# Kernel tuning notes

Hardware: AMD Instinct MI355X
Metric: run time of the kernel (lower is better)

The kernel has to match this reference:

```python
import jax, jax.numpy as jnp
import numpy as np

B, C, H, W_ = 16, 256, 128, 128

def setup_inputs() -> dict:
    key = jax.random.key(0)
    k1, k2 = jax.random.split(key)
    x = jax.random.normal(k1, (B, C, H, W_), dtype=jnp.float32)
    # nn.Linear(C, C): weight [C, C], bias [C]
    Wm = jax.random.normal(k2, (C, C), dtype=jnp.float32) * (1.0 / np.sqrt(C))
    b = jnp.zeros((C,), dtype=jnp.float32)
    return {"x": x, "W": Wm, "b": b}

def reference(x, W, b):
    # Channel frequency transform: mean of real(fft2) over spatial freq bins -> [B, C]
    cf = jnp.fft.fft2(x, axes=(-2, -1)).real.mean(axis=(-2, -1))
    cf = jax.nn.sigmoid(cf @ W.T + b)                       # [B, C]
    x_cft = x * cf[:, :, None, None]
    # Spatial frequency transform: fft2 of channel-mean map -> [B, H, W]
    sf = jnp.fft.fft2(x.mean(axis=1, keepdims=True), axes=(-2, -1)).real.mean(axis=1)
    x_sft = x * sf[:, None, :, :]
    return x_cft + x_sft
```

## Files before the change

### kernel.cpp

```cpp
#include <hip/hip_runtime.h>

#define Bn   16
#define Cn   256
#define Hd   128
#define Wd   128
#define HW   16384
#define HW4  4096

#define TWO_PI 6.283185307179586

#define OFF_XM   0
#define OFF_X00  262144
#define OFF_CF   266240
#define OFF_C1   270336
#define OFF_S1   532480
#define OFF_SF   794624

__global__ void k1_mean_x00(const float* __restrict__ x,
                            float* __restrict__ xm, float* __restrict__ x00) {
    int tid = blockIdx.x * blockDim.x + threadIdx.x;
    int b = tid >> 12;
    int p = tid & (HW4 - 1);
    const float4* base = (const float4*)x + (size_t)b * Cn * HW4 + p;
    float4 s = {0.f, 0.f, 0.f, 0.f};
    bool isp0 = (p == 0);
    #pragma unroll 4
    for (int c = 0; c < Cn; ++c) {
        float4 v = base[(size_t)c * HW4];
        s.x += v.x; s.y += v.y; s.z += v.z; s.w += v.w;
        if (isp0) x00[b * Cn + c] = v.x;
    }
    const float inv = 1.0f / (float)Cn;
    float4 o = { s.x * inv, s.y * inv, s.z * inv, s.w * inv };
    ((float4*)xm)[(size_t)b * HW4 + p] = o;
}

__global__ void k2_cf(const float* __restrict__ x00, const float* __restrict__ Wm,
                      const float* __restrict__ bias, float* __restrict__ cf) {
    __shared__ float xs[Cn];
    int b = blockIdx.x, c = threadIdx.x;
    xs[c] = x00[b * Cn + c];
    __syncthreads();
    float acc = bias[c];
    const float* wr = Wm + (size_t)c * Cn;
    #pragma unroll 8
    for (int k = 0; k < Cn; ++k) acc = fmaf(xs[k], wr[k], acc);
    cf[b * Cn + c] = 1.0f / (1.0f + expf(-acc));
}

__global__ void k3a_rows(const float* __restrict__ xm,
                         float* __restrict__ C1, float* __restrict__ S1) {
    __shared__ float tc[Hd], ts[Hd];
    int k1 = blockIdx.x & (Hd - 1);
    int b  = blockIdx.x >> 7;
    int n2 = threadIdx.x;
    {
        double ang = (double)n2 * (TWO_PI / (double)Hd);
        tc[n2] = (float)cos(ang);
        ts[n2] = (float)sin(ang);
    }
    __syncthreads();
    float ac = 0.f, as = 0.f;
    const float* xb = xm + (size_t)b * HW + n2;
    #pragma unroll 8
    for (int n1 = 0; n1 < Hd; ++n1) {
        int idx = (k1 * n1) & (Hd - 1);
        float v = xb[(size_t)n1 * Wd];
        ac = fmaf(tc[idx], v, ac);
        as = fmaf(ts[idx], v, as);
    }
    C1[(size_t)b * HW + k1 * Wd + n2] = ac;
    S1[(size_t)b * HW + k1 * Wd + n2] = as;
}

__global__ void k3b_cols(const float* __restrict__ C1, const float* __restrict__ S1,
                         float* __restrict__ sf) {
    __shared__ float tc[Wd], ts[Wd], c1s[Wd], s1s[Wd];
    int k1 = blockIdx.x & (Hd - 1);
    int b  = blockIdx.x >> 7;
    int k2 = threadIdx.x;
    {
        double ang = (double)k2 * (TWO_PI / (double)Wd);
        tc[k2] = (float)cos(ang);
        ts[k2] = (float)sin(ang);
        size_t row = (size_t)b * HW + k1 * Wd + k2;
        c1s[k2] = C1[row];
        s1s[k2] = S1[row];
    }
    __syncthreads();
    float acc = 0.f;
    #pragma unroll 8
    for (int n2 = 0; n2 < Wd; ++n2) {
        int idx = (k2 * n2) & (Wd - 1);
        acc = fmaf(tc[idx],  c1s[n2], acc);
        acc = fmaf(-ts[idx], s1s[n2], acc);
    }
    sf[(size_t)b * HW + k1 * Wd + k2] = acc;
}

__global__ void k4_out(const float* __restrict__ x, const float* __restrict__ cf,
                       const float* __restrict__ sf, float* __restrict__ out) {
    const size_t n4 = (size_t)Bn * Cn * HW4;
    size_t stride = (size_t)gridDim.x * blockDim.x;
    for (size_t i = (size_t)blockIdx.x * blockDim.x + threadIdx.x; i < n4; i += stride) {
        size_t e = i << 2;
        int b   = (int)(e >> 22);
        int c   = (int)((e >> 14) & (Cn - 1));
        int hw4 = (int)(i & (HW4 - 1));
        float cfv = cf[b * Cn + c];
        float4 sv = ((const float4*)sf)[(size_t)b * HW4 + hw4];
        float4 xv = ((const float4*)x)[i];
        float4 o;
        o.x = xv.x * (cfv + sv.x);
        o.y = xv.y * (cfv + sv.y);
        o.z = xv.z * (cfv + sv.z);
        o.w = xv.w * (cfv + sv.w);
        ((float4*)out)[i] = o;
    }
}

extern "C" void kernel_launch(void* const* d_in, const int* in_sizes, int n_in,
                              void* d_out, int out_size, void* d_ws, size_t ws_size,
                              hipStream_t stream) {
    const float* x    = (const float*)d_in[0];
    const float* Wm   = (const float*)d_in[1];
    const float* bias = (const float*)d_in[2];
    float* out = (float*)d_out;
    float* ws  = (float*)d_ws;

    float* xm  = ws + OFF_XM;
    float* x00 = ws + OFF_X00;
    float* cf  = ws + OFF_CF;
    float* C1  = ws + OFF_C1;
    float* S1  = ws + OFF_S1;
    float* sf  = ws + OFF_SF;

    k1_mean_x00<<<(Bn * HW4) / 256, 256, 0, stream>>>(x, xm, x00);
    k2_cf<<<Bn, Cn, 0, stream>>>(x00, Wm, bias, cf);
    k3a_rows<<<Bn * Hd, Wd, 0, stream>>>(xm, C1, S1);
    k3b_cols<<<Bn * Hd, Wd, 0, stream>>>(C1, S1, sf);
    k4_out<<<2048, 256, 0, stream>>>(x, cf, sf, out);
}
```

Before: 598.7 us.

## Split channel-mean reduction across channel chunks with a separate reduce kernel

The channel-mean kernel is split into a partial-sum pass over 8 channel chunks, launched with eight times as many threads, and a small reduction pass that combines the partials. The aim is more memory-level parallelism on the large streaming read of x, since the original launched too few threads, each looping serially over all 256 channels. The partial sums are staged in the output buffer, which the final kernel overwrites. This adds an extra launch and a small extra round trip to global memory.

```diff
diff --git a/kernel.cpp b/kernel.cpp
--- a/kernel.cpp
+++ b/kernel.cpp
@@ -6,6 +6,9 @@
 #define Wd   128
 #define HW   16384
 #define HW4  4096
+
+#define SPLIT 8
+#define CPS  (Cn / SPLIT)
 
 #define TWO_PI 6.283185307179586
 
@@ -16,19 +19,33 @@
 #define OFF_S1   532480
 #define OFF_SF   794624
 
-__global__ void k1_mean_x00(const float* __restrict__ x,
-                            float* __restrict__ xm, float* __restrict__ x00) {
+__global__ void k1a_partial(const float* __restrict__ x, float* __restrict__ part,
+                            float* __restrict__ x00) {
+    int tid = blockIdx.x * blockDim.x + threadIdx.x;
+    int p = tid & (HW4 - 1);
+    int b = (tid >> 12) & (Bn - 1);
+    int s = tid >> 16;
+    const float4* base = (const float4*)x + (size_t)b * Cn * HW4 + (size_t)s * CPS * HW4 + p;
+    float4 acc = {0.f, 0.f, 0.f, 0.f};
+    bool isp0 = (p == 0);
+    #pragma unroll
+    for (int c = 0; c < CPS; ++c) {
+        float4 v = base[(size_t)c * HW4];
+        acc.x += v.x; acc.y += v.y; acc.z += v.z; acc.w += v.w;
+        if (isp0) x00[b * Cn + s * CPS + c] = v.x;
+    }
+    ((float4*)part)[((size_t)s * Bn + b) * HW4 + p] = acc;
+}
+
+__global__ void k1b_reduce(const float* __restrict__ part, float* __restrict__ xm) {
     int tid = blockIdx.x * blockDim.x + threadIdx.x;
     int b = tid >> 12;
     int p = tid & (HW4 - 1);
-    const float4* base = (const float4*)x + (size_t)b * Cn * HW4 + p;
     float4 s = {0.f, 0.f, 0.f, 0.f};
-    bool isp0 = (p == 0);
-    #pragma unroll 4
-    for (int c = 0; c < Cn; ++c) {
-        float4 v = base[(size_t)c * HW4];
+    #pragma unroll
+    for (int k = 0; k < SPLIT; ++k) {
+        float4 v = ((const float4*)part)[((size_t)k * Bn + b) * HW4 + p];
         s.x += v.x; s.y += v.y; s.z += v.z; s.w += v.w;
-        if (isp0) x00[b * Cn + c] = v.x;
     }
     const float inv = 1.0f / (float)Cn;
     float4 o = { s.x * inv, s.y * inv, s.z * inv, s.w * inv };
@@ -134,8 +151,10 @@
     float* C1  = ws + OFF_C1;
     float* S1  = ws + OFF_S1;
     float* sf  = ws + OFF_SF;
+    float* part = out;
 
-    k1_mean_x00<<<(Bn * HW4) / 256, 256, 0, stream>>>(x, xm, x00);
+    k1a_partial<<<(Bn * HW4 * SPLIT) / 256, 256, 0, stream>>>(x, part, x00);
+    k1b_reduce<<<(Bn * HW4) / 256, 256, 0, stream>>>(part, xm);
     k2_cf<<<Bn, Cn, 0, stream>>>(x00, Wm, bias, cf);
     k3a_rows<<<Bn * Hd, Wd, 0, stream>>>(xm, C1, S1);
     k3b_cols<<<Bn * Hd, Wd, 0, stream>>>(C1, S1, sf);
```

Result: faster. 541.8 us (-9.5%).
